# Kernel tuning notes

Measured on AMD Instinct MI355X. Metric: run time of the kernel, lower is better.

Reference implementation:

```python
import jax, jax.numpy as jnp
import numpy as np

B, S, D = 2, 2048, 1024
H, DK = 16, 64
DFF = 4096
WINDOW = 128
GLOBAL = 16
EPS = 1e-5


def _layer_norm(x, g, b):
    mu = jnp.mean(x, axis=-1, keepdims=True)
    var = jnp.var(x, axis=-1, keepdims=True)
    return (x - mu) * jax.lax.rsqrt(var + EPS) * g + b


def setup_inputs() -> dict:
    key = jax.random.key(0)
    ks = jax.random.split(key, 12)
    s = 0.02
    inp = {
        "x": jax.random.normal(ks[0], (B, S, D), dtype=jnp.float32),
        "Wq": jax.random.normal(ks[1], (D, D), jnp.float32) * s,
        "bq": jnp.zeros((D,), jnp.float32),
        "Wk": jax.random.normal(ks[2], (D, D), jnp.float32) * s,
        "bk": jnp.zeros((D,), jnp.float32),
        "Wv": jax.random.normal(ks[3], (D, D), jnp.float32) * s,
        "bv": jnp.zeros((D,), jnp.float32),
        "Wo": jax.random.normal(ks[4], (D, D), jnp.float32) * s,
        "bo": jnp.zeros((D,), jnp.float32),
        "ln1_g": jnp.ones((D,), jnp.float32),
        "ln1_b": jnp.zeros((D,), jnp.float32),
        "W1": jax.random.normal(ks[5], (D, DFF), jnp.float32) * s,
        "b1": jnp.zeros((DFF,), jnp.float32),
        "W2": jax.random.normal(ks[6], (DFF, D), jnp.float32) * s,
        "b2": jnp.zeros((D,), jnp.float32),
        "ln2_g": jnp.ones((D,), jnp.float32),
        "ln2_b": jnp.zeros((D,), jnp.float32),
    }
    return inp


def _local_global_mask(seq_len):
    # token i attends to j iff |i-j| <= WINDOW, or i < GLOBAL, or j < GLOBAL
    i = jnp.arange(seq_len)[:, None]
    j = jnp.arange(seq_len)[None, :]
    m = jnp.abs(i - j) <= WINDOW
    m = m | (i < GLOBAL) | (j < GLOBAL)
    return m  # [S, S] bool


def reference(x, Wq, bq, Wk, bk, Wv, bv, Wo, bo, ln1_g, ln1_b,
              W1, b1, W2, b2, ln2_g, ln2_b):
    # --- self-attention sublayer (pre-norm residual) ---
    xn = _layer_norm(x, ln1_g, ln1_b)
    q = (xn @ Wq + bq).reshape(B, S, H, DK).transpose(0, 2, 1, 3)  # [B,H,S,DK]
    k = (xn @ Wk + bk).reshape(B, S, H, DK).transpose(0, 2, 1, 3)
    v = (xn @ Wv + bv).reshape(B, S, H, DK).transpose(0, 2, 1, 3)

    scores = jnp.einsum('bhqd,bhkd->bhqk', q, k) / jnp.sqrt(jnp.float32(DK))
    mask = _local_global_mask(S)  # [S,S]
    scores = jnp.where(mask[None, None], scores, jnp.float32(-jnp.inf))
    attn = jax.nn.softmax(scores, axis=-1)
    out = jnp.einsum('bhqk,bhkd->bhqd', attn, v)
    out = out.transpose(0, 2, 1, 3).reshape(B, S, D)
    out = out @ Wo + bo
    x = x + out

    # --- feed-forward sublayer (pre-norm residual) ---
    xn2 = _layer_norm(x, ln2_g, ln2_b)
    h = jax.nn.gelu(xn2 @ W1 + b1, approximate=False)
    ff = h @ W2 + b2
    x = x + ff
    return x
```

## Files before the change

### kernel.cpp

```cpp
#include <hip/hip_runtime.h>
#include <stdint.h>


typedef unsigned short u16;
typedef unsigned int   u32;
typedef __attribute__((ext_vector_type(8))) short  short8;
typedef __attribute__((ext_vector_type(4))) float  f32x4;

#define S_LEN   2048
#define D_MODEL 1024
#define ROWS    4096

__device__ __forceinline__ float bf2f(u16 u) {
  union { u32 i; float f; } v; v.i = ((u32)u) << 16; return v.f;
}
__device__ __forceinline__ float bflo(u32 u) {
  union { u32 i; float f; } v; v.i = u << 16; return v.f;
}
__device__ __forceinline__ float bfhi(u32 u) {
  union { u32 i; float f; } v; v.i = u & 0xffff0000u; return v.f;
}
__device__ __forceinline__ u16 f2bf(float f) {
  union { float f; u32 i; } v; v.f = f;
  u32 r = v.i + 0x7fffu + ((v.i >> 16) & 1u);
  return (u16)(r >> 16);
}

__device__ __forceinline__ void gld_lds16(const u16* g, u16* l) {
  __attribute__((address_space(3))) u32* lp =
      reinterpret_cast<__attribute__((address_space(3))) u32*>(
          reinterpret_cast<uintptr_t>(l));
  const __attribute__((address_space(1))) u32* gp =
      reinterpret_cast<const __attribute__((address_space(1))) u32*>(
          reinterpret_cast<uintptr_t>(g));
  __builtin_amdgcn_global_load_lds(gp, lp, 16, 0, 0);
}


#define GBAR  asm volatile("s_barrier" ::: "memory")
#define LGKM(n) asm volatile("s_waitcnt lgkmcnt(" #n ")" ::: "memory")
#define VM(n)   asm volatile("s_waitcnt vmcnt(" #n ")" ::: "memory")
#define SB0   __builtin_amdgcn_sched_barrier(0)

#define STAGE_A(buf, t, hm) do {                                              \
    gld_lds16(pA##hm + (size_t)(t) * 64,      &Ald[buf][0][(hm)*4096 + ldst]);\
    gld_lds16(pA##hm + (size_t)(t) * 64 + 32, &Ald[buf][1][(hm)*4096 + ldst]);\
  } while (0)

#define STAGE_B(buf, t, hm) do {                                              \
    gld_lds16(pB##hm + (size_t)(t) * 64,      &Bld[buf][0][(hm)*4096 + ldst]);\
    gld_lds16(pB##hm + (size_t)(t) * 64 + 32, &Bld[buf][1][(hm)*4096 + ldst]);\
  } while (0)

#define READ_B(buf) do {                                                      \
    _Pragma("unroll") for (int nj = 0; nj < 4; ++nj) {                        \
      bfv[nj][0] = *(const short8*)&Bld[buf][0][brow + nj * 512];             \
      bfv[nj][1] = *(const short8*)&Bld[buf][1][brow + nj * 512]; }           \
  } while (0)

#define READ_A(buf, q) do {                                                   \
    af[(q)&1][0][0] = *(const short8*)&Ald[buf][0][arow + (2*(q)) * 512];     \
    af[(q)&1][0][1] = *(const short8*)&Ald[buf][1][arow + (2*(q)) * 512];     \
    af[(q)&1][1][0] = *(const short8*)&Ald[buf][0][arow + (2*(q)+1) * 512];   \
    af[(q)&1][1][1] = *(const short8*)&Ald[buf][1][arow + (2*(q)+1) * 512];   \
  } while (0)

#define MFMA_Q(q) do {                                                        \
    __builtin_amdgcn_s_setprio(1);                                            \
    _Pragma("unroll") for (int dm = 0; dm < 2; ++dm)                          \
    _Pragma("unroll") for (int kk = 0; kk < 2; ++kk)                          \
    _Pragma("unroll") for (int nj = 0; nj < 4; ++nj)                          \
      acc[2*(q)+dm][nj] = __builtin_amdgcn_mfma_f32_16x16x32_bf16(            \
          af[(q)&1][dm][kk], bfv[nj][kk], acc[2*(q)+dm][nj], 0, 0, 0);        \
    __builtin_amdgcn_s_setprio(0);                                            \
  } while (0)

template <int EPI, int KC, int LDK>
__global__ __launch_bounds__(512) void gemm256(
    const u16* __restrict__ A, const u16* __restrict__ Bt,
    const float* __restrict__ bias, u16* __restrict__ C0,
    u16* __restrict__ C1, u16* __restrict__ C2, u16* __restrict__ C3,
    int N)
{
  __shared__ __attribute__((aligned(16))) u16 Ald[2][2][256 * 32];
  __shared__ __attribute__((aligned(16))) u16 Bld[2][2][256 * 32];

  const int tid  = threadIdx.x;
  const int w    = tid >> 6;
  const int lane = tid & 63;
  const int wm   = w >> 2;
  const int wn   = w & 3;
  const int lm   = lane & 15;
  const int kq   = lane >> 4;
  const int bm   = blockIdx.y * 256;
  const int bn   = blockIdx.x * 256;
  const int kz   = blockIdx.z;

  const u16* Ak = A  + (size_t)kz * KC;
  const u16* Bk = Bt + (size_t)kz * KC;
  u16* C = (kz == 0) ? C0 : (kz == 1) ? C1 : (kz == 2) ? C2 : C3;

  const int rslot = ((kq + (lm >> 1)) & 3) * 8;
  const int arow  = (wm * 128 + lm) * 32 + rslot;
  const int brow  = (wn * 64  + lm) * 32 + rslot;

  const int gcoff = (((lane & 3) - (lane >> 3)) & 3) * 8;
  const int srow  = w * 16 + (lane >> 2);
  const int ldst  = w * 512;

  const u16* pA0 = Ak + (size_t)(bm + srow) * LDK + gcoff;
  const u16* pA1 = pA0 + (size_t)128 * LDK;
  const u16* pB0 = Bk + (size_t)(bn + srow) * LDK + gcoff;
  const u16* pB1 = pB0 + (size_t)128 * LDK;

  f32x4 acc[8][4];
#pragma unroll
  for (int i = 0; i < 8; ++i)
#pragma unroll
    for (int j = 0; j < 4; ++j) acc[i][j] = (f32x4){0.f, 0.f, 0.f, 0.f};

  short8 af[2][2][2];
  short8 bfv[4][2];

  constexpr int P = KC >> 7;

  STAGE_B(0, 0, 0); STAGE_B(0, 0, 1);
  STAGE_A(0, 0, 0); STAGE_A(0, 0, 1);
  STAGE_B(1, 1, 0); STAGE_B(1, 1, 1);
  VM(4);
  GBAR;
  READ_A(0, 0);

  for (int i = 0; i < P - 1; ++i) {
    const int t1 = 2 * i + 1, t2 = 2 * i + 2, t3 = 2 * i + 3;
    GBAR; STAGE_A(1, t1, 0); READ_B(0); READ_A(0, 1); LGKM(4); SB0; MFMA_Q(0);
    GBAR; STAGE_A(1, t1, 1); READ_A(0, 2);            LGKM(4); SB0; MFMA_Q(1);
    GBAR; STAGE_B(0, t2, 0); READ_A(0, 3);            LGKM(4); SB0; MFMA_Q(2);
    VM(2);
    GBAR; STAGE_B(0, t2, 1); READ_A(1, 0);            LGKM(4); SB0; MFMA_Q(3);
    GBAR; STAGE_A(0, t2, 0); READ_B(1); READ_A(1, 1); LGKM(4); SB0; MFMA_Q(0);
    GBAR; STAGE_A(0, t2, 1); READ_A(1, 2);            LGKM(4); SB0; MFMA_Q(1);
    GBAR; STAGE_B(1, t3, 0); READ_A(1, 3);            LGKM(4); SB0; MFMA_Q(2);
    VM(2);
    GBAR; STAGE_B(1, t3, 1); READ_A(0, 0);            LGKM(4); SB0; MFMA_Q(3);
  }
  {
    const int t1 = 2 * P - 1;
    GBAR; STAGE_A(1, t1, 0); READ_B(0); READ_A(0, 1); LGKM(4); SB0; MFMA_Q(0);
    GBAR; STAGE_A(1, t1, 1); READ_A(0, 2);            LGKM(4); SB0; MFMA_Q(1);
    GBAR;                    READ_A(0, 3);            LGKM(4); SB0; MFMA_Q(2);
    VM(0);
    GBAR;                    READ_A(1, 0);            LGKM(4); SB0; MFMA_Q(3);
    GBAR;                    READ_B(1); READ_A(1, 1); LGKM(4); SB0; MFMA_Q(0);
    GBAR;                    READ_A(1, 2);            LGKM(4); SB0; MFMA_Q(1);
    GBAR;                    READ_A(1, 3);            LGKM(4); SB0; MFMA_Q(2);
    LGKM(0); SB0; MFMA_Q(3);
  }

  const int r0 = kq * 4;
#pragma unroll
  for (int mi = 0; mi < 8; ++mi) {
#pragma unroll
    for (int r = 0; r < 4; ++r) {
      const int grow = bm + wm * 128 + mi * 16 + r0 + r;
#pragma unroll
      for (int nj = 0; nj < 4; ++nj) {
        const int gcol = bn + wn * 64 + nj * 16 + lm;
        float v = acc[mi][nj][r];
        if (EPI < 2) v += bias[gcol];
        if (EPI == 1) v = 0.5f * v * (1.0f + erff(v * 0.70710678118654752f));
        C[(size_t)grow * N + gcol] = f2bf(v);
      }
    }
  }
}

__global__ __launch_bounds__(256) void reduce2(
    const u16* __restrict__ P0, const u16* __restrict__ P1,
    const float* __restrict__ bias, const float* res, float* out)
{
  const size_t base = ((size_t)blockIdx.x * 256 + threadIdx.x) * 8;
  const int col = (int)(base & 1023);
  uint4 p0 = *(const uint4*)(P0 + base);
  uint4 p1 = *(const uint4*)(P1 + base);
  float4 b0 = *(const float4*)(bias + col);
  float4 b1 = *(const float4*)(bias + col + 4);
  float4 r0 = *(const float4*)(res + base);
  float4 r1 = *(const float4*)(res + base + 4);
  float4 o0, o1;
  o0.x = bflo(p0.x) + bflo(p1.x) + b0.x + r0.x;
  o0.y = bfhi(p0.x) + bfhi(p1.x) + b0.y + r0.y;
  o0.z = bflo(p0.y) + bflo(p1.y) + b0.z + r0.z;
  o0.w = bfhi(p0.y) + bfhi(p1.y) + b0.w + r0.w;
  o1.x = bflo(p0.z) + bflo(p1.z) + b1.x + r1.x;
  o1.y = bfhi(p0.z) + bfhi(p1.z) + b1.y + r1.y;
  o1.z = bflo(p0.w) + bflo(p1.w) + b1.z + r1.z;
  o1.w = bfhi(p0.w) + bfhi(p1.w) + b1.w + r1.w;
  *(float4*)(out + base) = o0;
  *(float4*)(out + base + 4) = o1;
}

__global__ __launch_bounds__(256) void reduce4_ln(
    const u16* __restrict__ P0, const u16* __restrict__ P1,
    const u16* __restrict__ P2, const u16* __restrict__ P3,
    const float* __restrict__ bias, const float* __restrict__ res,
    const float* __restrict__ g, const float* __restrict__ bp,
    float* __restrict__ X1, u16* __restrict__ XN)
{
  const int row = blockIdx.x;
  const int t = threadIdx.x;
  const size_t base = (size_t)row * D_MODEL + t * 4;
  const int col = t * 4;
  uint2 a0 = *(const uint2*)(P0 + base);
  uint2 a1 = *(const uint2*)(P1 + base);
  uint2 a2 = *(const uint2*)(P2 + base);
  uint2 a3 = *(const uint2*)(P3 + base);
  float4 bb = *(const float4*)(bias + col);
  float4 rr = *(const float4*)(res + base);
  float4 y;
  y.x = bflo(a0.x) + bflo(a1.x) + bflo(a2.x) + bflo(a3.x) + bb.x + rr.x;
  y.y = bfhi(a0.x) + bfhi(a1.x) + bfhi(a2.x) + bfhi(a3.x) + bb.y + rr.y;
  y.z = bflo(a0.y) + bflo(a1.y) + bflo(a2.y) + bflo(a3.y) + bb.z + rr.z;
  y.w = bfhi(a0.y) + bfhi(a1.y) + bfhi(a2.y) + bfhi(a3.y) + bb.w + rr.w;
  *(float4*)(X1 + base) = y;

  float s  = y.x + y.y + y.z + y.w;
  float ss = y.x * y.x + y.y * y.y + y.z * y.z + y.w * y.w;
#pragma unroll
  for (int off = 32; off > 0; off >>= 1) {
    s  += __shfl_down(s, off);
    ss += __shfl_down(ss, off);
  }
  __shared__ float sm[4], ssm[4], stat[2];
  if ((t & 63) == 0) { sm[t >> 6] = s; ssm[t >> 6] = ss; }
  __syncthreads();
  if (t == 0) {
    float S = sm[0] + sm[1] + sm[2] + sm[3];
    float SS = ssm[0] + ssm[1] + ssm[2] + ssm[3];
    float mu = S * (1.0f / 1024.0f);
    float var = SS * (1.0f / 1024.0f) - mu * mu;
    stat[0] = mu;
    stat[1] = rsqrtf(fmaxf(var, 0.0f) + 1e-5f);
  }
  __syncthreads();
  const float mu = stat[0], rstd = stat[1];
  float4 gg = *(const float4*)(g + col);
  float4 be = *(const float4*)(bp + col);
  u16 o0 = f2bf((y.x - mu) * rstd * gg.x + be.x);
  u16 o1 = f2bf((y.y - mu) * rstd * gg.y + be.y);
  u16 o2 = f2bf((y.z - mu) * rstd * gg.z + be.z);
  u16 o3 = f2bf((y.w - mu) * rstd * gg.w + be.w);
  uint2 wv;
  wv.x = (u32)o0 | ((u32)o1 << 16);
  wv.y = (u32)o2 | ((u32)o3 << 16);
  *(uint2*)(XN + base) = wv;
}

__global__ __launch_bounds__(256) void ln_kernel(
    const float* __restrict__ x, const float* __restrict__ g,
    const float* __restrict__ b, u16* __restrict__ o)
{
  const int row = blockIdx.x;
  const int t = threadIdx.x;
  float4 v = *(const float4*)(x + (size_t)row * D_MODEL + t * 4);
  float s  = v.x + v.y + v.z + v.w;
  float ss = v.x * v.x + v.y * v.y + v.z * v.z + v.w * v.w;
#pragma unroll
  for (int off = 32; off > 0; off >>= 1) {
    s  += __shfl_down(s, off);
    ss += __shfl_down(ss, off);
  }
  __shared__ float sm[4], ssm[4], stat[2];
  if ((t & 63) == 0) { sm[t >> 6] = s; ssm[t >> 6] = ss; }
  __syncthreads();
  if (t == 0) {
    float S = sm[0] + sm[1] + sm[2] + sm[3];
    float SS = ssm[0] + ssm[1] + ssm[2] + ssm[3];
    float mu = S * (1.0f / 1024.0f);
    float var = SS * (1.0f / 1024.0f) - mu * mu;
    stat[0] = mu;
    stat[1] = rsqrtf(fmaxf(var, 0.0f) + 1e-5f);
  }
  __syncthreads();
  const float mu = stat[0], rstd = stat[1];
  float4 gg = *(const float4*)(g + t * 4);
  float4 bb = *(const float4*)(b + t * 4);
  u16 o0 = f2bf((v.x - mu) * rstd * gg.x + bb.x);
  u16 o1 = f2bf((v.y - mu) * rstd * gg.y + bb.y);
  u16 o2 = f2bf((v.z - mu) * rstd * gg.z + bb.z);
  u16 o3 = f2bf((v.w - mu) * rstd * gg.w + bb.w);
  uint2 w;
  w.x = (u32)o0 | ((u32)o1 << 16);
  w.y = (u32)o2 | ((u32)o3 << 16);
  *(uint2*)(o + (size_t)row * D_MODEL + t * 4) = w;
}

__global__ __launch_bounds__(256) void attn_band(
    const u16* __restrict__ qkv, u16* __restrict__ out)
{
  const int t    = threadIdx.x;
  const int w    = t >> 6;
  const int lane = t & 63;
  const int m    = lane & 15;
  const int quad = lane >> 4;
  const int bh   = blockIdx.y;
  const int b    = bh >> 4, h = bh & 15;
  const int i0   = blockIdx.x * 64;
  const size_t bb = (size_t)b * S_LEN;

  __shared__ __attribute__((aligned(16))) u16 Ks[32 * 72];
  __shared__ __attribute__((aligned(16))) u16 Vt[64 * 40];
  __shared__ __attribute__((aligned(16))) u16 Ps[4][16 * 40];

  const u16* qrow = qkv + (bb + i0 + 16 * w + m) * 3072 + h * 64;
  const short8 aq0 = *(const short8*)(qrow + quad * 8);
  const short8 aq1 = *(const short8*)(qrow + 32 + quad * 8);

  f32x4 Ov[4];
#pragma unroll
  for (int td = 0; td < 4; ++td) Ov[td] = (f32x4){0.f, 0.f, 0.f, 0.f};
  float mP[4] = {-1e30f, -1e30f, -1e30f, -1e30f};
  float lS[4] = {0.f, 0.f, 0.f, 0.f};

  const int iB = i0 + 16 * w + quad * 4;

  const int lo = max(32, i0 - 128);
  const int hi = min(S_LEN, i0 + 192);
  const int nChunks = 1 + (hi - lo) / 32;

  const int skr = t >> 3;
  const int skc = (t & 7) * 8;

  for (int c = 0; c < nChunks; ++c) {
    const int j0 = (c == 0) ? 0 : lo + (c - 1) * 32;
    __syncthreads();
    {
      const u16* src = qkv + (bb + j0 + skr) * 3072 + 1024 + h * 64 + skc;
      uint4 kk = *(const uint4*)src;
      uint4 vv = *(const uint4*)(src + 1024);
      *(uint4*)&Ks[skr * 72 + skc] = kk;
      const u16 vs[8] = {
        (u16)(vv.x & 0xffffu), (u16)(vv.x >> 16),
        (u16)(vv.y & 0xffffu), (u16)(vv.y >> 16),
        (u16)(vv.z & 0xffffu), (u16)(vv.z >> 16),
        (u16)(vv.w & 0xffffu), (u16)(vv.w >> 16)};
#pragma unroll
      for (int i = 0; i < 8; ++i) Vt[(skc + i) * 40 + skr] = vs[i];
    }
    __syncthreads();

    const short8 b00 = *(const short8*)&Ks[m * 72 + quad * 8];
    const short8 b01 = *(const short8*)&Ks[m * 72 + 32 + quad * 8];
    const short8 b10 = *(const short8*)&Ks[(16 + m) * 72 + quad * 8];
    const short8 b11 = *(const short8*)&Ks[(16 + m) * 72 + 32 + quad * 8];
    f32x4 s0 = (f32x4){0.f, 0.f, 0.f, 0.f};
    f32x4 s1 = (f32x4){0.f, 0.f, 0.f, 0.f};
    s0 = __builtin_amdgcn_mfma_f32_16x16x32_bf16(aq0, b00, s0, 0, 0, 0);
    s0 = __builtin_amdgcn_mfma_f32_16x16x32_bf16(aq1, b01, s0, 0, 0, 0);
    s1 = __builtin_amdgcn_mfma_f32_16x16x32_bf16(aq0, b10, s1, 0, 0, 0);
    s1 = __builtin_amdgcn_mfma_f32_16x16x32_bf16(aq1, b11, s1, 0, 0, 0);

    const int jA = j0 + m, jB = j0 + 16 + m;
#pragma unroll
    for (int r = 0; r < 4; ++r) {
      const int iG = iB + r;
      const int da = iG - jA, db = iG - jB;
      s0[r] = ((jA < 16) || (da >= -128 && da <= 128)) ? s0[r] * 0.125f : -1e30f;
      s1[r] = ((jB < 16) || (db >= -128 && db <= 128)) ? s1[r] * 0.125f : -1e30f;
    }

    float al[4];
#pragma unroll
    for (int r = 0; r < 4; ++r) {
      float mx = fmaxf(s0[r], s1[r]);
      mx = fmaxf(mx, __shfl_xor(mx, 1, 16));
      mx = fmaxf(mx, __shfl_xor(mx, 2, 16));
      mx = fmaxf(mx, __shfl_xor(mx, 4, 16));
      mx = fmaxf(mx, __shfl_xor(mx, 8, 16));
      const float mn = fmaxf(mP[r], mx);
      al[r] = __expf(mP[r] - mn);
      mP[r] = mn;
      const float p0 = __expf(s0[r] - mn);
      const float p1 = __expf(s1[r] - mn);
      float ps = p0 + p1;
      ps += __shfl_xor(ps, 1, 16);
      ps += __shfl_xor(ps, 2, 16);
      ps += __shfl_xor(ps, 4, 16);
      ps += __shfl_xor(ps, 8, 16);
      lS[r] = lS[r] * al[r] + ps;
      Ps[w][(quad * 4 + r) * 40 + m]      = f2bf(p0);
      Ps[w][(quad * 4 + r) * 40 + 16 + m] = f2bf(p1);
    }
#pragma unroll
    for (int td = 0; td < 4; ++td)
#pragma unroll
      for (int r = 0; r < 4; ++r) Ov[td][r] *= al[r];

    const short8 pa = *(const short8*)&Ps[w][m * 40 + quad * 8];
#pragma unroll
    for (int td = 0; td < 4; ++td) {
      const short8 bv = *(const short8*)&Vt[(td * 16 + m) * 40 + quad * 8];
      Ov[td] = __builtin_amdgcn_mfma_f32_16x16x32_bf16(pa, bv, Ov[td], 0, 0, 0);
    }
  }

  if (i0 + 16 * w >= 16) {
    float inv[4];
#pragma unroll
    for (int r = 0; r < 4; ++r) inv[r] = 1.0f / lS[r];
#pragma unroll
    for (int td = 0; td < 4; ++td)
#pragma unroll
      for (int r = 0; r < 4; ++r)
        out[(bb + iB + r) * 1024 + h * 64 + td * 16 + m] =
            f2bf(Ov[td][r] * inv[r]);
  }
}

__global__ __launch_bounds__(256) void attn_gpart(
    const u16* __restrict__ qkv, float* __restrict__ Obuf,
    float* __restrict__ mbuf, float* __restrict__ lbuf)
{
  const int t    = threadIdx.x;
  const int w    = t >> 6;
  const int lane = t & 63;
  const int m    = lane & 15;
  const int quad = lane >> 4;
  const int kb   = blockIdx.x;
  const int bh   = blockIdx.y;
  const int b    = bh >> 4, h = bh & 15;
  const size_t bb = (size_t)b * S_LEN;

  __shared__ __attribute__((aligned(16))) u16 Ks[4][32 * 72];
  __shared__ __attribute__((aligned(16))) u16 Vt[4][64 * 40];
  __shared__ __attribute__((aligned(16))) u16 Ps[4][16 * 40];

  const u16* qrow = qkv + (bb + m) * 3072 + h * 64;
  const short8 aq0 = *(const short8*)(qrow + quad * 8);
  const short8 aq1 = *(const short8*)(qrow + 32 + quad * 8);

  f32x4 Ov[4];
#pragma unroll
  for (int td = 0; td < 4; ++td) Ov[td] = (f32x4){0.f, 0.f, 0.f, 0.f};
  float mP[4] = {-1e30f, -1e30f, -1e30f, -1e30f};
  float lS[4] = {0.f, 0.f, 0.f, 0.f};

  const int srow = lane >> 1;
  const int sd   = (lane & 1) * 32;

  for (int c = 0; c < 2; ++c) {
    const int j0 = kb * 256 + w * 64 + c * 32;
    {
      const u16* src = qkv + (bb + j0 + srow) * 3072 + 1024 + h * 64 + sd;
      uint4 k0 = *(const uint4*)(src);
      uint4 k1 = *(const uint4*)(src + 8);
      uint4 k2 = *(const uint4*)(src + 16);
      uint4 k3 = *(const uint4*)(src + 24);
      *(uint4*)&Ks[w][srow * 72 + sd]      = k0;
      *(uint4*)&Ks[w][srow * 72 + sd + 8]  = k1;
      *(uint4*)&Ks[w][srow * 72 + sd + 16] = k2;
      *(uint4*)&Ks[w][srow * 72 + sd + 24] = k3;
#pragma unroll
      for (int q4 = 0; q4 < 4; ++q4) {
        uint4 vv = *(const uint4*)(src + 1024 + q4 * 8);
        const u16 vs[8] = {
          (u16)(vv.x & 0xffffu), (u16)(vv.x >> 16),
          (u16)(vv.y & 0xffffu), (u16)(vv.y >> 16),
          (u16)(vv.z & 0xffffu), (u16)(vv.z >> 16),
          (u16)(vv.w & 0xffffu), (u16)(vv.w >> 16)};
#pragma unroll
        for (int i = 0; i < 8; ++i)
          Vt[w][(sd + q4 * 8 + i) * 40 + srow] = vs[i];
      }
    }

    const short8 b00 = *(const short8*)&Ks[w][m * 72 + quad * 8];
    const short8 b01 = *(const short8*)&Ks[w][m * 72 + 32 + quad * 8];
    const short8 b10 = *(const short8*)&Ks[w][(16 + m) * 72 + quad * 8];
    const short8 b11 = *(const short8*)&Ks[w][(16 + m) * 72 + 32 + quad * 8];
    f32x4 s0 = (f32x4){0.f, 0.f, 0.f, 0.f};
    f32x4 s1 = (f32x4){0.f, 0.f, 0.f, 0.f};
    s0 = __builtin_amdgcn_mfma_f32_16x16x32_bf16(aq0, b00, s0, 0, 0, 0);
    s0 = __builtin_amdgcn_mfma_f32_16x16x32_bf16(aq1, b01, s0, 0, 0, 0);
    s1 = __builtin_amdgcn_mfma_f32_16x16x32_bf16(aq0, b10, s1, 0, 0, 0);
    s1 = __builtin_amdgcn_mfma_f32_16x16x32_bf16(aq1, b11, s1, 0, 0, 0);

    float al[4];
#pragma unroll
    for (int r = 0; r < 4; ++r) {
      const float v0 = s0[r] * 0.125f, v1 = s1[r] * 0.125f;
      float mx = fmaxf(v0, v1);
      mx = fmaxf(mx, __shfl_xor(mx, 1, 16));
      mx = fmaxf(mx, __shfl_xor(mx, 2, 16));
      mx = fmaxf(mx, __shfl_xor(mx, 4, 16));
      mx = fmaxf(mx, __shfl_xor(mx, 8, 16));
      const float mn = fmaxf(mP[r], mx);
      al[r] = __expf(mP[r] - mn);
      mP[r] = mn;
      const float p0 = __expf(v0 - mn);
      const float p1 = __expf(v1 - mn);
      float ps = p0 + p1;
      ps += __shfl_xor(ps, 1, 16);
      ps += __shfl_xor(ps, 2, 16);
      ps += __shfl_xor(ps, 4, 16);
      ps += __shfl_xor(ps, 8, 16);
      lS[r] = lS[r] * al[r] + ps;
      Ps[w][(quad * 4 + r) * 40 + m]      = f2bf(p0);
      Ps[w][(quad * 4 + r) * 40 + 16 + m] = f2bf(p1);
    }
#pragma unroll
    for (int td = 0; td < 4; ++td)
#pragma unroll
      for (int r = 0; r < 4; ++r) Ov[td][r] *= al[r];

    const short8 pa = *(const short8*)&Ps[w][m * 40 + quad * 8];
#pragma unroll
    for (int td = 0; td < 4; ++td) {
      const short8 bv = *(const short8*)&Vt[w][(td * 16 + m) * 40 + quad * 8];
      Ov[td] = __builtin_amdgcn_mfma_f32_16x16x32_bf16(pa, bv, Ov[td], 0, 0, 0);
    }
  }

  const int p = kb * 4 + w;
  const size_t ob = ((size_t)(bh * 32 + p)) * 16 * 64;
#pragma unroll
  for (int td = 0; td < 4; ++td)
#pragma unroll
    for (int r = 0; r < 4; ++r)
      Obuf[ob + (size_t)(quad * 4 + r) * 64 + td * 16 + m] = Ov[td][r];
  if (m == 0) {
    const int mb = (bh * 32 + p) * 16;
#pragma unroll
    for (int r = 0; r < 4; ++r) {
      mbuf[mb + quad * 4 + r] = mP[r];
      lbuf[mb + quad * 4 + r] = lS[r];
    }
  }
}

__global__ __launch_bounds__(256) void attn_gcombine(
    const float* __restrict__ Obuf, const float* __restrict__ mbuf,
    const float* __restrict__ lbuf, u16* __restrict__ out)
{
  const int bh = blockIdx.x;
  const int b  = bh >> 4, h = bh & 15;
  const int t  = threadIdx.x;
  const int q  = t >> 4;
  const int d0 = (t & 15) * 4;
  const int mb = bh * 32 * 16;

  float mv[32];
  float M = -1e30f;
#pragma unroll
  for (int p = 0; p < 32; ++p) {
    mv[p] = mbuf[mb + p * 16 + q];
    M = fmaxf(M, mv[p]);
  }
  float L = 0.f;
  float4 acc = {0.f, 0.f, 0.f, 0.f};
#pragma unroll
  for (int p = 0; p < 32; ++p) {
    const float wp = __expf(mv[p] - M);
    L += lbuf[mb + p * 16 + q] * wp;
    float4 o = *(const float4*)&Obuf[(((size_t)(bh * 32 + p)) * 16 + q) * 64 + d0];
    acc.x += wp * o.x; acc.y += wp * o.y;
    acc.z += wp * o.z; acc.w += wp * o.w;
  }
  const float inv = 1.0f / L;
  uint2 wv;
  wv.x = (u32)f2bf(acc.x * inv) | ((u32)f2bf(acc.y * inv) << 16);
  wv.y = (u32)f2bf(acc.z * inv) | ((u32)f2bf(acc.w * inv) << 16);
  *(uint2*)(out + ((size_t)b * S_LEN + q) * 1024 + h * 64 + d0) = wv;
}

__global__ __launch_bounds__(256) void prep_all(
    const float* __restrict__ Wq, const float* __restrict__ Wk,
    const float* __restrict__ Wv, const float* __restrict__ Wo,
    const float* __restrict__ W1, const float* __restrict__ W2,
    const float* __restrict__ bq, const float* __restrict__ bk,
    const float* __restrict__ bv,
    u16* __restrict__ WQKVT, u16* __restrict__ WOT,
    u16* __restrict__ W1T, u16* __restrict__ W2T,
    float* __restrict__ BQKV)
{
  const int gb = blockIdx.x;
  const int t = threadIdx.x;
  if (gb >= 3072) {
    const int i = (gb - 3072) * 256 + t;
    if (i < 1024) BQKV[i] = bq[i];
    else if (i < 2048) BQKV[i] = bk[i - 1024];
    else BQKV[i] = bv[i - 2048];
    return;
  }
  const float* in; u16* outp; int R, Cc, bx, by;
  if (gb < 1024) {
    const int seg = gb >> 8, local = gb & 255;
    bx = local & 15; by = local >> 4; R = 1024; Cc = 1024;
    in   = (seg == 0) ? Wq : (seg == 1) ? Wk : (seg == 2) ? Wv : Wo;
    outp = (seg < 3) ? WQKVT + (size_t)seg * 1024 * 1024 : WOT;
  } else if (gb < 2048) {
    const int local = gb - 1024;
    bx = local & 63; by = local >> 6; R = 1024; Cc = 4096;
    in = W1; outp = W1T;
  } else {
    const int local = gb - 2048;
    bx = local & 15; by = local >> 4; R = 4096; Cc = 1024;
    in = W2; outp = W2T;
  }

  __shared__ u16 tile[64][65];
  const int tr = by * 64, tc = bx * 64;
  const int lr = t >> 2, lc0 = (t & 3) * 16;
  const float* src = in + (size_t)(tr + lr) * Cc + tc + lc0;
  float4 a0 = *(const float4*)(src);
  float4 a1 = *(const float4*)(src + 4);
  float4 a2 = *(const float4*)(src + 8);
  float4 a3 = *(const float4*)(src + 12);
  const float vals[16] = {a0.x, a0.y, a0.z, a0.w, a1.x, a1.y, a1.z, a1.w,
                          a2.x, a2.y, a2.z, a2.w, a3.x, a3.y, a3.z, a3.w};
#pragma unroll
  for (int q = 0; q < 16; ++q) tile[lr][lc0 + q] = f2bf(vals[q]);
  __syncthreads();
  u16* dst = outp + (size_t)(tc + lr) * R + tr + lc0;
  u32 w[8];
#pragma unroll
  for (int q = 0; q < 8; ++q)
    w[q] = (u32)tile[lc0 + 2 * q][lr] | ((u32)tile[lc0 + 2 * q + 1][lr] << 16);
  uint4 s0; s0.x = w[0]; s0.y = w[1]; s0.z = w[2]; s0.w = w[3];
  uint4 s1; s1.x = w[4]; s1.y = w[5]; s1.z = w[6]; s1.w = w[7];
  *(uint4*)dst = s0;
  *(uint4*)(dst + 8) = s1;
}

static const size_t OFF_WQKVT = 0;
static const size_t OFF_WOT   = OFF_WQKVT + (size_t)3072 * 1024 * 2;
static const size_t OFF_W1T   = OFF_WOT   + (size_t)1024 * 1024 * 2;
static const size_t OFF_W2T   = OFF_W1T   + (size_t)4096 * 1024 * 2;
static const size_t OFF_BQKV  = OFF_W2T   + (size_t)1024 * 4096 * 2;
static const size_t OFF_XN    = OFF_BQKV  + 16384;
static const size_t OFF_QKV   = OFF_XN    + (size_t)4096 * 1024 * 2;
static const size_t OFF_AO    = OFF_QKV   + (size_t)4096 * 3072 * 2;
static const size_t OFF_H     = OFF_QKV;

extern "C" void kernel_launch(void* const* d_in, const int* in_sizes, int n_in,
                              void* d_out, int out_size, void* d_ws, size_t ws_size,
                              hipStream_t stream)
{
  const float* x   = (const float*)d_in[0];
  const float* Wq  = (const float*)d_in[1];
  const float* bq  = (const float*)d_in[2];
  const float* Wk  = (const float*)d_in[3];
  const float* bk  = (const float*)d_in[4];
  const float* Wv  = (const float*)d_in[5];
  const float* bv  = (const float*)d_in[6];
  const float* Wo  = (const float*)d_in[7];
  const float* bo  = (const float*)d_in[8];
  const float* g1  = (const float*)d_in[9];
  const float* be1 = (const float*)d_in[10];
  const float* W1  = (const float*)d_in[11];
  const float* b1  = (const float*)d_in[12];
  const float* W2  = (const float*)d_in[13];
  const float* b2  = (const float*)d_in[14];
  const float* g2  = (const float*)d_in[15];
  const float* be2 = (const float*)d_in[16];
  float* outf = (float*)d_out;
  char* ws = (char*)d_ws;

  u16*   WQKVT = (u16*)(ws + OFF_WQKVT);
  u16*   WOT   = (u16*)(ws + OFF_WOT);
  u16*   W1T   = (u16*)(ws + OFF_W1T);
  u16*   W2T   = (u16*)(ws + OFF_W2T);
  float* BQKV  = (float*)(ws + OFF_BQKV);
  u16*   XN    = (u16*)(ws + OFF_XN);
  u16*   QKV   = (u16*)(ws + OFF_QKV);
  u16*   AO    = (u16*)(ws + OFF_AO);
  u16*   Hbuf  = (u16*)(ws + OFF_H);
  float* X1    = outf;
  u16* PWo0 = (u16*)(ws + OFF_QKV);
  u16* PWo1 = PWo0 + (size_t)4096 * 1024;
  u16* PWo2 = PWo1 + (size_t)4096 * 1024;
  u16* PWo3 = (u16*)(ws + OFF_XN);
  u16* PW20 = (u16*)(ws + OFF_W1T);
  u16* PW21 = (u16*)(ws + OFF_XN);
  float* GO = (float*)(ws + OFF_XN);
  float* GM = GO + (size_t)32 * 32 * 16 * 64;
  float* GL = GM + 32 * 32 * 16;

  const dim3 blk(256);
  const dim3 blk512(512);
  prep_all<<<dim3(3084), blk, 0, stream>>>(Wq, Wk, Wv, Wo, W1, W2, bq, bk, bv,
                                           WQKVT, WOT, W1T, W2T, BQKV);

  ln_kernel<<<dim3(ROWS), blk, 0, stream>>>(x, g1, be1, XN);
  gemm256<0, 1024, 1024><<<dim3(12, 16, 1), blk512, 0, stream>>>(
      XN, WQKVT, BQKV, QKV, QKV, QKV, QKV, 3072);
  attn_band<<<dim3(32, 32), blk, 0, stream>>>(QKV, AO);
  attn_gpart<<<dim3(8, 32), blk, 0, stream>>>(QKV, GO, GM, GL);
  attn_gcombine<<<dim3(32), blk, 0, stream>>>(GO, GM, GL, AO);
  gemm256<2, 256, 1024><<<dim3(4, 16, 4), blk512, 0, stream>>>(
      AO, WOT, nullptr, PWo0, PWo1, PWo2, PWo3, 1024);
  reduce4_ln<<<dim3(ROWS), blk, 0, stream>>>(PWo0, PWo1, PWo2, PWo3,
                                             bo, x, g2, be2, X1, XN);

  gemm256<1, 1024, 1024><<<dim3(16, 16, 1), blk512, 0, stream>>>(
      XN, W1T, b1, Hbuf, Hbuf, Hbuf, Hbuf, 4096);
  gemm256<2, 2048, 4096><<<dim3(4, 16, 2), blk512, 0, stream>>>(
      Hbuf, W2T, nullptr, PW20, PW21, PW21, PW21, 1024);
  reduce2<<<dim3(2048), blk, 0, stream>>>(PW20, PW21, b2, X1, outf);
}
```

Measured before the change: 348.2 us.

## Replace interleaved quarter-step GEMM pipeline with simple per-tile double buffering

The hand-scheduled 8-phase main loop is replaced with a simpler per-k-tile double-buffered loop. Before, LDS fragment reads, partial global-to-LDS staging and MFMA quarters were interleaved under explicit lgkmcnt waits and sched barriers. Now each iteration issues all loads for the next tile, waits for the current tile, then reads all fragments and runs all MFMAs, leaving instruction ordering to the compiler. This cuts barriers and code complexity per tile, but risks less overlap between LDS reads and MFMA issue.

```diff
diff --git a/kernel.cpp b/kernel.cpp
--- a/kernel.cpp
+++ b/kernel.cpp
@@ -36,11 +36,8 @@
   __builtin_amdgcn_global_load_lds(gp, lp, 16, 0, 0);
 }
 
-
 #define GBAR  asm volatile("s_barrier" ::: "memory")
-#define LGKM(n) asm volatile("s_waitcnt lgkmcnt(" #n ")" ::: "memory")
-#define VM(n)   asm volatile("s_waitcnt vmcnt(" #n ")" ::: "memory")
-#define SB0   __builtin_amdgcn_sched_barrier(0)
+#define VM(n) asm volatile("s_waitcnt vmcnt(" #n ")" ::: "memory")
 
 #define STAGE_A(buf, t, hm) do {                                              \
     gld_lds16(pA##hm + (size_t)(t) * 64,      &Ald[buf][0][(hm)*4096 + ldst]);\
@@ -52,27 +49,32 @@
     gld_lds16(pB##hm + (size_t)(t) * 64 + 32, &Bld[buf][1][(hm)*4096 + ldst]);\
   } while (0)
 
-#define READ_B(buf) do {                                                      \
+#define COMPUTE(rb) do {                                                      \
+    short8 bfv[4][2];                                                         \
     _Pragma("unroll") for (int nj = 0; nj < 4; ++nj) {                        \
-      bfv[nj][0] = *(const short8*)&Bld[buf][0][brow + nj * 512];             \
-      bfv[nj][1] = *(const short8*)&Bld[buf][1][brow + nj * 512]; }           \
+      bfv[nj][0] = *(const short8*)&Bld[rb][0][brow + nj * 512];              \
+      bfv[nj][1] = *(const short8*)&Bld[rb][1][brow + nj * 512]; }            \
+    __builtin_amdgcn_s_setprio(1);                                            \
+    _Pragma("unroll") for (int mi = 0; mi < 8; ++mi) {                        \
+      short8 a0 = *(const short8*)&Ald[rb][0][arow + mi * 512];               \
+      short8 a1 = *(const short8*)&Ald[rb][1][arow + mi * 512];               \
+      _Pragma("unroll") for (int nj = 0; nj < 4; ++nj)                        \
+        acc[mi][nj] = __builtin_amdgcn_mfma_f32_16x16x32_bf16(                \
+            a0, bfv[nj][0], acc[mi][nj], 0, 0, 0);                            \
+      _Pragma("unroll") for (int nj = 0; nj < 4; ++nj)                        \
+        acc[mi][nj] = __builtin_amdgcn_mfma_f32_16x16x32_bf16(                \
+            a1, bfv[nj][1], acc[mi][nj], 0, 0, 0);                            \
+    }                                                                         \
+    __builtin_amdgcn_s_setprio(0);                                            \
   } while (0)
 
-#define READ_A(buf, q) do {                                                   \
-    af[(q)&1][0][0] = *(const short8*)&Ald[buf][0][arow + (2*(q)) * 512];     \
-    af[(q)&1][0][1] = *(const short8*)&Ald[buf][1][arow + (2*(q)) * 512];     \
-    af[(q)&1][1][0] = *(const short8*)&Ald[buf][0][arow + (2*(q)+1) * 512];   \
-    af[(q)&1][1][1] = *(const short8*)&Ald[buf][1][arow + (2*(q)+1) * 512];   \
-  } while (0)
-
-#define MFMA_Q(q) do {                                                        \
-    __builtin_amdgcn_s_setprio(1);                                            \
-    _Pragma("unroll") for (int dm = 0; dm < 2; ++dm)                          \
-    _Pragma("unroll") for (int kk = 0; kk < 2; ++kk)                          \
-    _Pragma("unroll") for (int nj = 0; nj < 4; ++nj)                          \
-      acc[2*(q)+dm][nj] = __builtin_amdgcn_mfma_f32_16x16x32_bf16(            \
-          af[(q)&1][dm][kk], bfv[nj][kk], acc[2*(q)+dm][nj], 0, 0, 0);        \
-    __builtin_amdgcn_s_setprio(0);                                            \
+#define GTILE_MID(t, rb) do {                                                 \
+    GBAR;                                                                     \
+    STAGE_A((rb)^1, (t) + 1, 0); STAGE_A((rb)^1, (t) + 1, 1);                 \
+    STAGE_B((rb)^1, (t) + 1, 0); STAGE_B((rb)^1, (t) + 1, 1);                 \
+    VM(8);                                                                    \
+    GBAR;                                                                     \
+    COMPUTE(rb);                                                              \
   } while (0)
 
 template <int EPI, int KC, int LDK>
@@ -119,43 +121,27 @@
 #pragma unroll
     for (int j = 0; j < 4; ++j) acc[i][j] = (f32x4){0.f, 0.f, 0.f, 0.f};
 
-  short8 af[2][2][2];
-  short8 bfv[4][2];
-
-  constexpr int P = KC >> 7;
-
+  constexpr int NT = KC >> 6;
+
+  STAGE_A(0, 0, 0); STAGE_A(0, 0, 1);
   STAGE_B(0, 0, 0); STAGE_B(0, 0, 1);
-  STAGE_A(0, 0, 0); STAGE_A(0, 0, 1);
+  STAGE_A(1, 1, 0); STAGE_A(1, 1, 1);
   STAGE_B(1, 1, 0); STAGE_B(1, 1, 1);
-  VM(4);
+
+  VM(8);
   GBAR;
-  READ_A(0, 0);
-
-  for (int i = 0; i < P - 1; ++i) {
-    const int t1 = 2 * i + 1, t2 = 2 * i + 2, t3 = 2 * i + 3;
-    GBAR; STAGE_A(1, t1, 0); READ_B(0); READ_A(0, 1); LGKM(4); SB0; MFMA_Q(0);
-    GBAR; STAGE_A(1, t1, 1); READ_A(0, 2);            LGKM(4); SB0; MFMA_Q(1);
-    GBAR; STAGE_B(0, t2, 0); READ_A(0, 3);            LGKM(4); SB0; MFMA_Q(2);
-    VM(2);
-    GBAR; STAGE_B(0, t2, 1); READ_A(1, 0);            LGKM(4); SB0; MFMA_Q(3);
-    GBAR; STAGE_A(0, t2, 0); READ_B(1); READ_A(1, 1); LGKM(4); SB0; MFMA_Q(0);
-    GBAR; STAGE_A(0, t2, 1); READ_A(1, 2);            LGKM(4); SB0; MFMA_Q(1);
-    GBAR; STAGE_B(1, t3, 0); READ_A(1, 3);            LGKM(4); SB0; MFMA_Q(2);
-    VM(2);
-    GBAR; STAGE_B(1, t3, 1); READ_A(0, 0);            LGKM(4); SB0; MFMA_Q(3);
-  }
-  {
-    const int t1 = 2 * P - 1;
-    GBAR; STAGE_A(1, t1, 0); READ_B(0); READ_A(0, 1); LGKM(4); SB0; MFMA_Q(0);
-    GBAR; STAGE_A(1, t1, 1); READ_A(0, 2);            LGKM(4); SB0; MFMA_Q(1);
-    GBAR;                    READ_A(0, 3);            LGKM(4); SB0; MFMA_Q(2);
-    VM(0);
-    GBAR;                    READ_A(1, 0);            LGKM(4); SB0; MFMA_Q(3);
-    GBAR;                    READ_B(1); READ_A(1, 1); LGKM(4); SB0; MFMA_Q(0);
-    GBAR;                    READ_A(1, 2);            LGKM(4); SB0; MFMA_Q(1);
-    GBAR;                    READ_A(1, 3);            LGKM(4); SB0; MFMA_Q(2);
-    LGKM(0); SB0; MFMA_Q(3);
-  }
+  COMPUTE(0);
+
+#pragma unroll 1
+  for (int tp = 0; tp < (NT - 2) / 2; ++tp) {
+    GTILE_MID(1 + 2 * tp, 1);
+    GTILE_MID(2 + 2 * tp, 0);
+  }
+
+  GBAR;
+  VM(0);
+  GBAR;
+  COMPUTE(1);
 
   const int r0 = kq * 4;
 #pragma unroll
```

New measurement: 372.9 us. 7.1% more time.
